# Optimization experiments

Measured on AMD Instinct MI355X. Metric: run time of the kernel, lower is better.

Reference implementation:

```python
import jax, jax.numpy as jnp
import numpy as np
import math

B, S, HID = 2, 2048, 4096
NH, NKV = 32, 8
HD = HID // NH  # 128
ROPE_BASE = 10000.0


def _rope_tables(seq_len, dim, base=ROPE_BASE):
    # ntk_alpha = 1 and mscale = 1 for seq_len <= training_seqlen
    inv_freq = 1.0 / (base ** (jnp.arange(0, dim, 2, dtype=jnp.float32) / dim))
    t = jnp.arange(seq_len, dtype=jnp.float32)
    freqs = jnp.einsum('i,j->ij', t, inv_freq)          # [S, dim/2]
    emb = jnp.concatenate([freqs, freqs], axis=-1)       # [S, dim]
    return jnp.cos(emb), jnp.sin(emb)


def setup_inputs() -> dict:
    key = jax.random.key(0)
    ks = jax.random.split(key, 5)
    hidden_states = jax.random.normal(ks[0], (B, S, HID), dtype=jnp.float32)
    # additive causal mask [B, 1, S, S]
    causal = jnp.where(jnp.tril(jnp.ones((S, S), dtype=bool)), 0.0, -1e9)
    attention_mask = jnp.broadcast_to(causal[None, None], (B, 1, S, S)).astype(jnp.float32)
    cos, sin = _rope_tables(S, HD)
    sc = 0.02
    Wq = jax.random.normal(ks[1], (HID, HID), dtype=jnp.float32) * sc
    Wkv = jax.random.normal(ks[2], (2 * NKV * HD, HID), dtype=jnp.float32) * sc
    Wd = jax.random.normal(ks[3], (HID, HID), dtype=jnp.float32) * sc
    bd = jnp.zeros((HID,), dtype=jnp.float32)
    return {"hidden_states": hidden_states, "attention_mask": attention_mask,
            "cos": cos, "sin": sin, "Wq": Wq, "Wkv": Wkv, "Wd": Wd, "bd": bd}


def _rotate_half(x):
    x1, x2 = jnp.split(x, 2, axis=-1)
    return jnp.concatenate([-x2, x1], axis=-1)


def reference(hidden_states, attention_mask, cos, sin, Wq, Wkv, Wd, bd):
    bsz, seq_len, _ = hidden_states.shape
    # Q projection: [B,S,HID] -> [B,NH,S,HD]
    q = (hidden_states @ Wq.T).reshape(bsz, seq_len, NH, HD).transpose(0, 2, 1, 3)
    # fused KV projection: [B,S,NKV,2*HD] -> split -> [B,NKV,S,HD] each
    kv = (hidden_states @ Wkv.T).reshape(bsz, seq_len, NKV, 2 * HD)
    k, v = jnp.split(kv, 2, axis=-1)
    k = k.transpose(0, 2, 1, 3)
    v = v.transpose(0, 2, 1, 3)
    # RoPE (broadcast cos/sin [S,HD] over batch and heads)
    c = cos[None, None, :, :]
    s = sin[None, None, :, :]
    q = q * c + _rotate_half(q) * s
    k = k * c + _rotate_half(k) * s
    # repeat_kv: expand KV heads to NH heads (group size NH//NKV)
    n_rep = NH // NKV
    k = jnp.repeat(k, n_rep, axis=1)  # [B,NH,S,HD]
    v = jnp.repeat(v, n_rep, axis=1)
    # attention
    scores = jnp.einsum('bhqd,bhkd->bhqk', q, k) / math.sqrt(HD)
    scores = scores + attention_mask[:, :, :, :seq_len]
    probs = jax.nn.softmax(scores.astype(jnp.float32), axis=-1).astype(q.dtype)
    attn = jnp.einsum('bhqk,bhkd->bhqd', probs, v)
    attn = attn.transpose(0, 2, 1, 3).reshape(bsz, seq_len, HID)
    return attn @ Wd.T + bd
```

## Files before the change

### kernel.cpp

```cpp
#include <hip/hip_runtime.h>

typedef __bf16 bf16;
typedef __bf16 bf16x4 __attribute__((ext_vector_type(4)));
typedef __bf16 bf16x8 __attribute__((ext_vector_type(8)));
typedef float floatx4 __attribute__((ext_vector_type(4)));

static constexpr int B_ = 2, S_ = 2048, HID_ = 4096, NH_ = 32, NKV_ = 8, HD_ = 128;

__device__ __forceinline__ void gll16(const void* g, void* l) {
    __builtin_amdgcn_global_load_lds(
        (const __attribute__((address_space(1))) void*)g,
        (__attribute__((address_space(3))) void*)l, 16, 0, 0);
}

__device__ __forceinline__ bf16x8 cvt8(const float* p) {
    float4 f0 = *(const float4*)p;
    float4 f1 = *(const float4*)(p + 4);
    bf16x8 v;
    v[0] = (bf16)f0.x; v[1] = (bf16)f0.y; v[2] = (bf16)f0.z; v[3] = (bf16)f0.w;
    v[4] = (bf16)f1.x; v[5] = (bf16)f1.y; v[6] = (bf16)f1.z; v[7] = (bf16)f1.w;
    return v;
}

__global__ __launch_bounds__(256) void cvt_kernel(const float* __restrict__ in,
                                                  bf16* __restrict__ out, int n8)
{
    int i = blockIdx.x * 256 + threadIdx.x;
    if (i >= n8) return;
    ((bf16x8*)out)[i] = cvt8(in + (size_t)i * 8);
}

template<int EPI>
__global__ __launch_bounds__(512, 2) void gemm256_kernel(
    const bf16* __restrict__ Ap, const bf16* __restrict__ Wp,
    const float* __restrict__ bias, void* __restrict__ Cp,
    bf16* __restrict__ Kw, bf16* __restrict__ Vtw,
    int M, int N, int K)
{
    __shared__ __attribute__((aligned(16))) bf16 As[4 * 8192];
    __shared__ __attribute__((aligned(16))) bf16 Bs[4 * 8192];

    const int tid = threadIdx.x;
    const int lane = tid & 63, wv = tid >> 6;
    const int lm = lane & 15, lq = lane >> 4;
    const int wr = (wv >> 2) * 128, wc = (wv & 3) * 64;
    const int m0 = blockIdx.y * 256, n0 = blockIdx.x * 256;

    const int NT = K >> 5;

    const int sr = lane >> 2, sch = lane & 3;
    const bf16* aA0 = Ap + (size_t)(m0 + wv * 32 +      sr) * K + sch * 8;
    const bf16* aA1 = Ap + (size_t)(m0 + wv * 32 + 16 + sr) * K + sch * 8;
    const bf16* aB0 = Wp + (size_t)(n0 + wv * 32 +      sr) * K + sch * 8;
    const bf16* aB1 = Wp + (size_t)(n0 + wv * 32 + 16 + sr) * K + sch * 8;
    const int ub0 = wv * 1024;
    const int ub1 = wv * 1024 + 512;

    floatx4 acc[8][4];
    #pragma unroll
    for (int i = 0; i < 8; i++)
        #pragma unroll
        for (int j = 0; j < 4; j++) acc[i][j] = (floatx4){0.f, 0.f, 0.f, 0.f};

    #pragma unroll
    for (int ts = 0; ts < 3; ++ts) {
        if (ts < NT) {
            const int sl = ts & 3;
            const size_t ko = (size_t)ts * 32;
            gll16(aA0 + ko, &As[sl * 8192 + ub0]);
            gll16(aA1 + ko, &As[sl * 8192 + ub1]);
            gll16(aB0 + ko, &Bs[sl * 8192 + ub0]);
            gll16(aB1 + ko, &Bs[sl * 8192 + ub1]);
        }
    }
    if (NT >= 3) asm volatile("s_waitcnt vmcnt(8)");
    else         asm volatile("s_waitcnt vmcnt(0)");
    __builtin_amdgcn_s_barrier();

    for (int t = 0; t < NT; ++t) {
        const bf16* Asl = As + (t & 3) * 8192;
        const bf16* Bsl = Bs + (t & 3) * 8192;
        const int ts = t + 3;
        const int sl = ts & 3;
        const bool st = ts < NT;
        const size_t ko = (size_t)ts * 32;

        bf16x8 af[4], bfr[4];
        #pragma unroll
        for (int i = 0; i < 4; i++)
            af[i] = *(const bf16x8*)&Asl[(wr + i * 16 + lm) * 32 + lq * 8];
        #pragma unroll
        for (int j = 0; j < 4; j++)
            bfr[j] = *(const bf16x8*)&Bsl[(wc + j * 16 + lm) * 32 + lq * 8];
        if (st) {
            gll16(aA0 + ko, &As[sl * 8192 + ub0]);
            gll16(aA1 + ko, &As[sl * 8192 + ub1]);
        }
        __builtin_amdgcn_s_barrier();
        asm volatile("s_waitcnt lgkmcnt(0)");
        __builtin_amdgcn_s_setprio(1);
        #pragma unroll
        for (int i = 0; i < 4; i++)
            #pragma unroll
            for (int j = 0; j < 4; j++)
                acc[i][j] = __builtin_amdgcn_mfma_f32_16x16x32_bf16(af[i], bfr[j], acc[i][j], 0, 0, 0);
        __builtin_amdgcn_s_setprio(0);
        __builtin_amdgcn_s_barrier();

        bf16x8 af2[4];
        #pragma unroll
        for (int i = 0; i < 4; i++)
            af2[i] = *(const bf16x8*)&Asl[(wr + 64 + i * 16 + lm) * 32 + lq * 8];
        if (st) {
            gll16(aB0 + ko, &Bs[sl * 8192 + ub0]);
            gll16(aB1 + ko, &Bs[sl * 8192 + ub1]);
        }
        __builtin_amdgcn_s_barrier();
        asm volatile("s_waitcnt lgkmcnt(0)");
        __builtin_amdgcn_s_setprio(1);
        #pragma unroll
        for (int i = 0; i < 4; i++)
            #pragma unroll
            for (int j = 0; j < 4; j++)
                acc[4 + i][j] = __builtin_amdgcn_mfma_f32_16x16x32_bf16(af2[i], bfr[j], acc[4 + i][j], 0, 0, 0);
        __builtin_amdgcn_s_setprio(0);
        if (t < NT - 3)       asm volatile("s_waitcnt vmcnt(8)");
        else if (t == NT - 3) asm volatile("s_waitcnt vmcnt(4)");
        else                  asm volatile("s_waitcnt vmcnt(0)");
        __builtin_amdgcn_s_barrier();
    }

    #pragma unroll
    for (int i = 0; i < 8; i++)
        #pragma unroll
        for (int j = 0; j < 4; j++) {
            const int col = n0 + wc + j * 16 + lm;
            const int row0 = m0 + wr + i * 16 + lq * 4;
            if (EPI == 0) {
                #pragma unroll
                for (int r = 0; r < 4; r++)
                    ((bf16*)Cp)[(size_t)(row0 + r) * N + col] = (bf16)acc[i][j][r];
            } else if (EPI == 1) {
                const float bv = bias ? bias[col] : 0.f;
                #pragma unroll
                for (int r = 0; r < 4; r++)
                    ((float*)Cp)[(size_t)(row0 + r) * N + col] = acc[i][j][r] + bv;
            } else {
                const int head = col >> 8, off = col & 255;
                const int b = row0 >> 11, s0 = row0 & (S_ - 1);
                if (off < HD_) {
                    bf16* kp = Kw + ((size_t)(b * NKV_ + head) * S_ + s0) * HD_ + off;
                    #pragma unroll
                    for (int r = 0; r < 4; r++) kp[(size_t)r * HD_] = (bf16)acc[i][j][r];
                } else {
                    bf16x4 pv;
                    #pragma unroll
                    for (int r = 0; r < 4; r++) pv[r] = (bf16)acc[i][j][r];
                    *(bf16x4*)&Vtw[((size_t)(b * NKV_ + head) * HD_ + (off - HD_)) * S_ + s0] = pv;
                }
            }
        }
}

template<bool ABF, bool WBF, int EPI>
__global__ __launch_bounds__(256) void gemm_kernel(
    const void* __restrict__ Ap, const void* __restrict__ Wp,
    const float* __restrict__ bias, void* __restrict__ Cp,
    bf16* __restrict__ Kw, bf16* __restrict__ Vtw,
    int M, int N, int K)
{
    constexpr bool FAST = ABF && WBF;
    constexpr int STR = FAST ? 32 : 40;
    __shared__ __attribute__((aligned(16))) bf16 smem[2 * 128 * 40];
    bf16* Als = smem;
    bf16* Bls = smem + 128 * STR;

    const int tid = threadIdx.x;
    const int lane = tid & 63, wave = tid >> 6;
    const int lm = lane & 15, lq = lane >> 4;
    const int wr = (wave >> 1) * 64, wc = (wave & 1) * 64;
    const int m0 = blockIdx.y * 128, n0 = blockIdx.x * 128;

    floatx4 acc[4][4];
    #pragma unroll
    for (int i = 0; i < 4; i++)
        #pragma unroll
        for (int j = 0; j < 4; j++) acc[i][j] = (floatx4){0.f, 0.f, 0.f, 0.f};

    const int sr = tid >> 1;
    const int sc = (tid & 1) * 16;

    for (int k0 = 0; k0 < K; k0 += 32) {
        __syncthreads();
        if (FAST) {
            #pragma unroll
            for (int t = 0; t < 2; t++) {
                const int o = wave * 2048 + t * 1024 + lane * 16;
                const int row = o >> 6, ch = (o >> 4) & 3;
                const int ub = wave * 1024 + t * 512;
                gll16((const bf16*)Ap + (size_t)(m0 + row) * K + k0 + ch * 8, &Als[ub]);
                gll16((const bf16*)Wp + (size_t)(n0 + row) * K + k0 + ch * 8, &Bls[ub]);
            }
        } else {
            if (ABF) {
                const bf16* aptr = (const bf16*)Ap + (size_t)(m0 + sr) * K + sc + k0;
                *(bf16x8*)&Als[sr * STR + sc]     = *(const bf16x8*)(aptr);
                *(bf16x8*)&Als[sr * STR + sc + 8] = *(const bf16x8*)(aptr + 8);
            } else {
                const float* aptr = (const float*)Ap + (size_t)(m0 + sr) * K + sc + k0;
                *(bf16x8*)&Als[sr * STR + sc]     = cvt8(aptr);
                *(bf16x8*)&Als[sr * STR + sc + 8] = cvt8(aptr + 8);
            }
            const float* wptr = (const float*)Wp + (size_t)(n0 + sr) * K + sc + k0;
            *(bf16x8*)&Bls[sr * STR + sc]     = cvt8(wptr);
            *(bf16x8*)&Bls[sr * STR + sc + 8] = cvt8(wptr + 8);
        }
        __syncthreads();
        bf16x8 af[4], bfr[4];
        const int ko = lq * 8;
        #pragma unroll
        for (int i = 0; i < 4; i++) af[i]  = *(const bf16x8*)&Als[(wr + i * 16 + lm) * STR + ko];
        #pragma unroll
        for (int j = 0; j < 4; j++) bfr[j] = *(const bf16x8*)&Bls[(wc + j * 16 + lm) * STR + ko];
        #pragma unroll
        for (int i = 0; i < 4; i++)
            #pragma unroll
            for (int j = 0; j < 4; j++)
                acc[i][j] = __builtin_amdgcn_mfma_f32_16x16x32_bf16(af[i], bfr[j], acc[i][j], 0, 0, 0);
    }

    #pragma unroll
    for (int i = 0; i < 4; i++)
        #pragma unroll
        for (int j = 0; j < 4; j++) {
            const int col = n0 + wc + j * 16 + lm;
            const int row0 = m0 + wr + i * 16 + lq * 4;
            if (EPI == 0) {
                #pragma unroll
                for (int r = 0; r < 4; r++)
                    ((bf16*)Cp)[(size_t)(row0 + r) * N + col] = (bf16)acc[i][j][r];
            } else if (EPI == 1) {
                const float bv = bias ? bias[col] : 0.f;
                #pragma unroll
                for (int r = 0; r < 4; r++)
                    ((float*)Cp)[(size_t)(row0 + r) * N + col] = acc[i][j][r] + bv;
            } else {
                const int head = col >> 8, off = col & 255;
                const int b = row0 >> 11, s0 = row0 & (S_ - 1);
                if (off < HD_) {
                    bf16* kp = Kw + ((size_t)(b * NKV_ + head) * S_ + s0) * HD_ + off;
                    #pragma unroll
                    for (int r = 0; r < 4; r++) kp[(size_t)r * HD_] = (bf16)acc[i][j][r];
                } else {
                    bf16x4 pv;
                    #pragma unroll
                    for (int r = 0; r < 4; r++) pv[r] = (bf16)acc[i][j][r];
                    *(bf16x4*)&Vtw[((size_t)(b * NKV_ + head) * HD_ + (off - HD_)) * S_ + s0] = pv;
                }
            }
        }
}

__global__ __launch_bounds__(256) void rope_kernel(
    bf16* __restrict__ Qd, bf16* __restrict__ Kd,
    const float* __restrict__ cosd, const float* __restrict__ sind)
{
    const int idx = blockIdx.x * 256 + threadIdx.x;
    const int QROWS = B_ * S_ * NH_;
    const int d = idx & 63;
    const int row = idx >> 6;
    bf16* base; int s;
    if (row < QROWS) { base = Qd + (size_t)row * HD_; s = (row / NH_) & (S_ - 1); }
    else            { int rk = row - QROWS; base = Kd + (size_t)rk * HD_; s = rk & (S_ - 1); }
    const float c  = cosd[s * HD_ + d];
    const float sn = sind[s * HD_ + d];
    const float x1 = (float)base[d];
    const float x2 = (float)base[d + 64];
    base[d]      = (bf16)(x1 * c - x2 * sn);
    base[d + 64] = (bf16)(x2 * c + x1 * sn);
}

__global__ __launch_bounds__(256) void attn_kernel(
    const bf16* __restrict__ Q, const bf16* __restrict__ Kw,
    const bf16* __restrict__ Vtw, bf16* __restrict__ O)
{
    const int bq = (int)gridDim.x - 1 - (int)blockIdx.x;
    const int h = blockIdx.y, b = blockIdx.z;
    const int kh = h >> 2;
    const int tid = threadIdx.x, wave = tid >> 6, lane = tid & 63;
    const int lm = lane & 15, lq = lane >> 4;

    __shared__ __attribute__((aligned(16))) bf16 Kls[64 * 128];
    __shared__ __attribute__((aligned(16))) bf16 Vls[128 * 64];
    __shared__ __attribute__((aligned(16))) bf16 Pls[4][16 * 72];

    const int q0 = bq * 64 + wave * 16;
    bf16x8 qa[4];
    {
        const bf16* qb = Q + ((size_t)(b * S_ + q0 + lm) * NH_ + h) * HD_;
        #pragma unroll
        for (int ks = 0; ks < 4; ks++) qa[ks] = *(const bf16x8*)(qb + ks * 32 + lq * 8);
    }

    float l_i[4];
    floatx4 oacc[8];
    #pragma unroll
    for (int r = 0; r < 4; r++) l_i[r] = 0.f;
    #pragma unroll
    for (int ct = 0; ct < 8; ct++) oacc[ct] = (floatx4){0.f, 0.f, 0.f, 0.f};

    const float scale = 0.08838834764831845f;
    const bf16* Kbase = Kw  + (size_t)(b * NKV_ + kh) * S_ * HD_;
    const bf16* Vbase = Vtw + (size_t)(b * NKV_ + kh) * HD_ * S_;
    const int nkt = bq + 1;

    for (int it = 0; it < nkt; ++it) {
        const int kt = it * 64;
        __syncthreads();
        #pragma unroll
        for (int t = 0; t < 4; t++) {
            const int o = wave * 4096 + t * 1024 + lane * 16;
            const int ub = (wave * 4096 + t * 1024) / 2;
            { const int row = o >> 8, pos = (o >> 4) & 15, c = (pos - row) & 15;
              gll16(Kbase + (size_t)(kt + row) * HD_ + c * 8, &Kls[ub]); }
            { const int row = o >> 7, pos = (o >> 4) & 7, c = (pos - row) & 7;
              gll16(Vbase + (size_t)row * S_ + kt + c * 8, &Vls[ub]); }
        }
        __syncthreads();

        floatx4 sacc[4];
        #pragma unroll
        for (int nt = 0; nt < 4; nt++) sacc[nt] = (floatx4){0.f, 0.f, 0.f, 0.f};
        #pragma unroll
        for (int nt = 0; nt < 4; nt++) {
            const int key = nt * 16 + lm;
            #pragma unroll
            for (int ks = 0; ks < 4; ks++) {
                bf16x8 kf = *(const bf16x8*)&Kls[key * 128 + ((ks * 4 + lq + key) & 15) * 8];
                sacc[nt] = __builtin_amdgcn_mfma_f32_16x16x32_bf16(qa[ks], kf, sacc[nt], 0, 0, 0);
            }
        }

        #pragma unroll
        for (int r = 0; r < 4; r++) {
            const int qrow = q0 + lq * 4 + r;
            float lacc = 0.f;
            #pragma unroll
            for (int nt = 0; nt < 4; nt++) {
                const int kcol = kt + nt * 16 + lm;
                const float sv = sacc[nt][r] * scale + (kcol > qrow ? -1e9f : 0.f);
                const float p = __expf(sv - 20.0f);
                lacc += p;
                Pls[wave][(lq * 4 + r) * 72 + nt * 16 + lm] = (bf16)p;
            }
            l_i[r] += lacc;
        }

        #pragma unroll
        for (int ks2 = 0; ks2 < 2; ks2++) {
            bf16x8 pa = *(const bf16x8*)&Pls[wave][lm * 72 + ks2 * 32 + lq * 8];
            #pragma unroll
            for (int ct = 0; ct < 8; ct++) {
                const int dr = ct * 16 + lm;
                bf16x8 vb = *(const bf16x8*)&Vls[dr * 64 + ((ks2 * 4 + lq + dr) & 7) * 8];
                oacc[ct] = __builtin_amdgcn_mfma_f32_16x16x32_bf16(pa, vb, oacc[ct], 0, 0, 0);
            }
        }
    }

    #pragma unroll
    for (int r = 0; r < 4; r++) {
        float l = l_i[r];
        #pragma unroll
        for (int off = 1; off < 16; off <<= 1)
            l += __shfl_xor(l, off, 64);
        l_i[r] = l;
    }

    #pragma unroll
    for (int ct = 0; ct < 8; ct++)
        #pragma unroll
        for (int r = 0; r < 4; r++) {
            const int qrow = q0 + lq * 4 + r;
            O[(size_t)(b * S_ + qrow) * HID_ + h * HD_ + ct * 16 + lm]
                = (bf16)(oacc[ct][r] / l_i[r]);
        }
}

extern "C" void kernel_launch(void* const* d_in, const int* in_sizes, int n_in,
                              void* d_out, int out_size, void* d_ws, size_t ws_size,
                              hipStream_t stream)
{
    const float* hidden = (const float*)d_in[0];
    const float* cosd = (const float*)d_in[2];
    const float* sind = (const float*)d_in[3];
    const float* Wq   = (const float*)d_in[4];
    const float* Wkv  = (const float*)d_in[5];
    const float* Wd   = (const float*)d_in[6];
    const float* bd   = (const float*)d_in[7];
    float* out = (float*)d_out;

    const int M = B_ * S_;
    const int NKVC = 2 * NKV_ * HD_;
    bf16* Qw = (bf16*)d_out;
    bf16* wsb = (bf16*)d_ws;
    dim3 blk(256);
    dim3 blk512(512);

    const size_t E_HID  = (size_t)M * HID_;
    const size_t E_WKV  = (size_t)NKVC * HID_;
    const size_t E_K    = (size_t)B_ * NKV_ * S_ * HD_;
    const bool full = ws_size >= 2 * (3 * E_HID + E_WKV + 2 * E_K);

    const int rope_blocks = (B_ * S_ * NH_ + B_ * NKV_ * S_) * 64 / 256;

    if (full) {
        bf16* hb   = wsb;
        bf16* wqb  = hb   + E_HID;
        bf16* wkvb = wqb  + E_HID;
        bf16* wdb  = wkvb + E_WKV;
        bf16* Kw   = wdb  + E_HID;
        bf16* Vtw  = Kw   + E_K;
        bf16* Aw   = hb;

        cvt_kernel<<<dim3(E_HID / 8 / 256), blk, 0, stream>>>(hidden, hb,  (int)(E_HID / 8));
        cvt_kernel<<<dim3(E_HID / 8 / 256), blk, 0, stream>>>(Wq,     wqb, (int)(E_HID / 8));
        cvt_kernel<<<dim3(E_WKV / 8 / 256), blk, 0, stream>>>(Wkv,    wkvb,(int)(E_WKV / 8));
        cvt_kernel<<<dim3(E_HID / 8 / 256), blk, 0, stream>>>(Wd,     wdb, (int)(E_HID / 8));

        gemm256_kernel<0><<<dim3(HID_ / 256, M / 256), blk512, 0, stream>>>(
            hb, wqb, nullptr, Qw, nullptr, nullptr, M, HID_, HID_);
        gemm256_kernel<2><<<dim3(NKVC / 256, M / 256), blk512, 0, stream>>>(
            hb, wkvb, nullptr, nullptr, Kw, Vtw, M, NKVC, HID_);
        rope_kernel<<<dim3(rope_blocks), blk, 0, stream>>>(Qw, Kw, cosd, sind);
        attn_kernel<<<dim3(S_ / 64, NH_, B_), blk, 0, stream>>>(Qw, Kw, Vtw, Aw);
        gemm256_kernel<1><<<dim3(HID_ / 256, M / 256), blk512, 0, stream>>>(
            Aw, wdb, bd, out, nullptr, nullptr, M, HID_, HID_);
    } else {
        bf16* Kw  = wsb;
        bf16* Vtw = Kw  + E_K;
        bf16* Aw  = Vtw + E_K;

        gemm_kernel<false, false, 0><<<dim3(HID_ / 128, M / 128), blk, 0, stream>>>(
            hidden, Wq, nullptr, Qw, nullptr, nullptr, M, HID_, HID_);
        gemm_kernel<false, false, 2><<<dim3(NKVC / 128, M / 128), blk, 0, stream>>>(
            hidden, Wkv, nullptr, nullptr, Kw, Vtw, M, NKVC, HID_);
        rope_kernel<<<dim3(rope_blocks), blk, 0, stream>>>(Qw, Kw, cosd, sind);
        attn_kernel<<<dim3(S_ / 64, NH_, B_), blk, 0, stream>>>(Qw, Kw, Vtw, Aw);
        gemm_kernel<true, false, 1><<<dim3(HID_ / 128, M / 128), blk, 0, stream>>>(
            Aw, Wd, bd, out, nullptr, nullptr, M, HID_, HID_);
    }
}
```

Baseline: 888.8 us.

## Swizzle GEMM LDS tiles and double-buffer K/V loads in attention

The GEMM kernel applies an XOR swizzle to the 16-byte chunk index when writing and reading the A/B LDS tiles, to cut LDS bank conflicts on the fragment reads. The attention kernel double-buffers its K and V LDS tiles, issuing the next tile's global-to-LDS loads before computing on the current one, which replaces the two syncthreads per iteration with a single wait and barrier. It also raises wave priority around the MFMA blocks. This doubles the attention LDS footprint, which may lower occupancy.

```diff
diff --git a/kernel.cpp b/kernel.cpp
--- a/kernel.cpp
+++ b/kernel.cpp
@@ -48,13 +48,16 @@
 
     const int NT = K >> 5;
 
-    const int sr = lane >> 2, sch = lane & 3;
+    const int sr = lane >> 2;
+    const int sch = (lane & 3) ^ ((lane >> 3) & 3);
     const bf16* aA0 = Ap + (size_t)(m0 + wv * 32 +      sr) * K + sch * 8;
     const bf16* aA1 = Ap + (size_t)(m0 + wv * 32 + 16 + sr) * K + sch * 8;
     const bf16* aB0 = Wp + (size_t)(n0 + wv * 32 +      sr) * K + sch * 8;
     const bf16* aB1 = Wp + (size_t)(n0 + wv * 32 + 16 + sr) * K + sch * 8;
     const int ub0 = wv * 1024;
     const int ub1 = wv * 1024 + 512;
+
+    const int rko = (lq ^ ((lm >> 1) & 3)) * 8;
 
     floatx4 acc[8][4];
     #pragma unroll
@@ -88,10 +91,10 @@
         bf16x8 af[4], bfr[4];
         #pragma unroll
         for (int i = 0; i < 4; i++)
-            af[i] = *(const bf16x8*)&Asl[(wr + i * 16 + lm) * 32 + lq * 8];
+            af[i] = *(const bf16x8*)&Asl[(wr + i * 16 + lm) * 32 + rko];
         #pragma unroll
         for (int j = 0; j < 4; j++)
-            bfr[j] = *(const bf16x8*)&Bsl[(wc + j * 16 + lm) * 32 + lq * 8];
+            bfr[j] = *(const bf16x8*)&Bsl[(wc + j * 16 + lm) * 32 + rko];
         if (st) {
             gll16(aA0 + ko, &As[sl * 8192 + ub0]);
             gll16(aA1 + ko, &As[sl * 8192 + ub1]);
@@ -110,7 +113,7 @@
         bf16x8 af2[4];
         #pragma unroll
         for (int i = 0; i < 4; i++)
-            af2[i] = *(const bf16x8*)&Asl[(wr + 64 + i * 16 + lm) * 32 + lq * 8];
+            af2[i] = *(const bf16x8*)&Asl[(wr + 64 + i * 16 + lm) * 32 + rko];
         if (st) {
             gll16(aB0 + ko, &Bs[sl * 8192 + ub0]);
             gll16(aB1 + ko, &Bs[sl * 8192 + ub1]);
@@ -290,8 +293,8 @@
     const int tid = threadIdx.x, wave = tid >> 6, lane = tid & 63;
     const int lm = lane & 15, lq = lane >> 4;
 
-    __shared__ __attribute__((aligned(16))) bf16 Kls[64 * 128];
-    __shared__ __attribute__((aligned(16))) bf16 Vls[128 * 64];
+    __shared__ __attribute__((aligned(16))) bf16 Kls[2 * 64 * 128];
+    __shared__ __attribute__((aligned(16))) bf16 Vls[2 * 128 * 64];
     __shared__ __attribute__((aligned(16))) bf16 Pls[4][16 * 72];
 
     const int q0 = bq * 64 + wave * 16;
@@ -314,32 +317,44 @@
     const bf16* Vbase = Vtw + (size_t)(b * NKV_ + kh) * HD_ * S_;
     const int nkt = bq + 1;
 
-    for (int it = 0; it < nkt; ++it) {
+    auto stage = [&](int it, int slot) {
         const int kt = it * 64;
-        __syncthreads();
         #pragma unroll
         for (int t = 0; t < 4; t++) {
             const int o = wave * 4096 + t * 1024 + lane * 16;
-            const int ub = (wave * 4096 + t * 1024) / 2;
+            const int ub = (wave * 4096 + t * 1024) / 2 + slot * 8192;
             { const int row = o >> 8, pos = (o >> 4) & 15, c = (pos - row) & 15;
               gll16(Kbase + (size_t)(kt + row) * HD_ + c * 8, &Kls[ub]); }
             { const int row = o >> 7, pos = (o >> 4) & 7, c = (pos - row) & 7;
               gll16(Vbase + (size_t)row * S_ + kt + c * 8, &Vls[ub]); }
         }
-        __syncthreads();
+    };
+
+    stage(0, 0);
+    asm volatile("s_waitcnt vmcnt(0)" ::: "memory");
+    __builtin_amdgcn_s_barrier();
+
+    for (int it = 0; it < nkt; ++it) {
+        const int kt = it * 64;
+        const int cur = it & 1;
+        if (it + 1 < nkt) stage(it + 1, cur ^ 1);
+        const bf16* Kc = Kls + cur * 8192;
+        const bf16* Vc = Vls + cur * 8192;
 
         floatx4 sacc[4];
         #pragma unroll
         for (int nt = 0; nt < 4; nt++) sacc[nt] = (floatx4){0.f, 0.f, 0.f, 0.f};
+        __builtin_amdgcn_s_setprio(1);
         #pragma unroll
         for (int nt = 0; nt < 4; nt++) {
             const int key = nt * 16 + lm;
             #pragma unroll
             for (int ks = 0; ks < 4; ks++) {
-                bf16x8 kf = *(const bf16x8*)&Kls[key * 128 + ((ks * 4 + lq + key) & 15) * 8];
+                bf16x8 kf = *(const bf16x8*)&Kc[key * 128 + ((ks * 4 + lq + key) & 15) * 8];
                 sacc[nt] = __builtin_amdgcn_mfma_f32_16x16x32_bf16(qa[ks], kf, sacc[nt], 0, 0, 0);
             }
         }
+        __builtin_amdgcn_s_setprio(0);
 
         #pragma unroll
         for (int r = 0; r < 4; r++) {
@@ -356,16 +371,21 @@
             l_i[r] += lacc;
         }
 
+        __builtin_amdgcn_s_setprio(1);
         #pragma unroll
         for (int ks2 = 0; ks2 < 2; ks2++) {
             bf16x8 pa = *(const bf16x8*)&Pls[wave][lm * 72 + ks2 * 32 + lq * 8];
             #pragma unroll
             for (int ct = 0; ct < 8; ct++) {
                 const int dr = ct * 16 + lm;
-                bf16x8 vb = *(const bf16x8*)&Vls[dr * 64 + ((ks2 * 4 + lq + dr) & 7) * 8];
+                bf16x8 vb = *(const bf16x8*)&Vc[dr * 64 + ((ks2 * 4 + lq + dr) & 7) * 8];
                 oacc[ct] = __builtin_amdgcn_mfma_f32_16x16x32_bf16(pa, vb, oacc[ct], 0, 0, 0);
             }
         }
+        __builtin_amdgcn_s_setprio(0);
+
+        asm volatile("s_waitcnt vmcnt(0)" ::: "memory");
+        __builtin_amdgcn_s_barrier();
     }
 
     #pragma unroll
```

Result: no change. 891.8 us (+0.3%).
